# Kernel tuning notes

Hardware: AMD Instinct MI355X
Metric: run time of the kernel (lower is better)

The kernel has to match this reference:

```python
import jax, jax.numpy as jnp
import numpy as np

NUM_GROUPS = 512   # G: number of FPS centers
GROUP_SIZE = 32    # K: neighbors per group


def setup_inputs() -> dict:
    key = jax.random.key(0)
    points = jax.random.normal(key, (16, 8192, 6), dtype=jnp.float32)  # [B,N,C], xyz = first 3 ch
    return {"points": points}


def _farthest_point_sampling(xyz, K):
    """Iterative FPS. xyz: [B,N,3] -> indices [B,K] (int32).

    Deterministic start at index 0 (the torch module uses a random start; we fix
    it for a reproducible reference -- the math per step is identical).
    """
    B, N, _ = xyz.shape
    start = jnp.zeros((B,), dtype=jnp.int32)
    min_d = jnp.full((B, N), jnp.inf, dtype=xyz.dtype)

    def step(carry, _):
        min_d, last = carry
        last_pt = jnp.take_along_axis(xyz, last[:, None, None], axis=1)  # [B,1,3]
        d = jnp.sum((xyz - last_pt) ** 2, axis=-1)                       # [B,N]
        min_d = jnp.minimum(min_d, d)
        nxt = jnp.argmax(min_d, axis=-1).astype(jnp.int32)
        return (min_d, nxt), last

    _, idxs = jax.lax.scan(step, (min_d, start), None, length=K)
    return jnp.transpose(idxs)  # [B,K]


def reference(points):
    xyz = points[:, :, :3]                                   # [B,N,3]
    fps_idx = _farthest_point_sampling(xyz, NUM_GROUPS)      # [B,G]
    centers = jnp.take_along_axis(xyz, fps_idx[:, :, None], axis=1)  # [B,G,3]

    # Squared pairwise distances [B,G,N] via expanded GEMM (compute-dominant part).
    d2 = (jnp.sum(centers * centers, axis=-1)[:, :, None]
          - 2.0 * jnp.einsum('bgc,bnc->bgn', centers, xyz)
          + jnp.sum(xyz * xyz, axis=-1)[:, None, :])

    # KNN: smallest K distances (torch uses return_sorted=False; ordering of the
    # K neighbors is irrelevant to the grouping semantics).
    _, knn_idx = jax.lax.top_k(-d2, GROUP_SIZE)              # [B,G,K]

    # knn_gather: [B,N,C] gathered by [B,G,K] -> [B,G,K,C]
    grouped = jax.vmap(lambda p, i: p[i])(points, knn_idx)

    # Center-subtract on xyz channels only.
    grouped = jnp.concatenate(
        [grouped[..., :3] - centers[:, :, None, :], grouped[..., 3:]], axis=-1)
    return grouped, centers
```

## Files before the change

### kernel.cpp

```cpp
#include <hip/hip_runtime.h>
#include <hip/hip_bf16.h>
#include <stdint.h>

#define BATCH 16
#define NPTS  8192
#define NCH   6
#define NGRP  512
#define GSZ   32

#define FPS_T   1024
#define FPS_PPT 8
#define FPS_W   16

typedef float v2f __attribute__((ext_vector_type(2)));

template <int CTRL>
__device__ __forceinline__ float dpp_max_f32(float v) {
  const int t =
      __builtin_amdgcn_update_dpp(0, __float_as_int(v), CTRL, 0xf, 0xf, true);
  return fmaxf(v, __int_as_float(t));
}

template <int CTRL>
__device__ __forceinline__ unsigned dpp_min_u32(unsigned v) {
  const int t = __builtin_amdgcn_update_dpp((int)0xFFFFFFFF, (int)v, CTRL,
                                            0xf, 0xf, false);
  const unsigned tu = (unsigned)t;
  return v < tu ? v : tu;
}

__global__ __launch_bounds__(FPS_T, 1) void fps_kernel(
    const float* __restrict__ points, float* __restrict__ centers) {
#pragma clang fp contract(off)
  const int b    = blockIdx.x;
  const int tid  = threadIdx.x;
  const int lane = tid & 63;
  const int wave = tid >> 6;
  const float* P = points + (size_t)b * NPTS * NCH;
  float* C = centers + (size_t)b * NGRP * 3;

  __shared__ float cache[NPTS * 3];
  __shared__ unsigned long long wslot[2][FPS_W];

  v2f px[4], py[4], pz[4], md[4];
  {
    float* fx = (float*)px; float* fy = (float*)py; float* fz = (float*)pz;
#pragma unroll
    for (int j = 0; j < FPS_PPT; ++j) {
      const int i = tid * FPS_PPT + j;
      const float x = P[i * 6 + 0];
      const float y = P[i * 6 + 1];
      const float z = P[i * 6 + 2];
      fx[j] = x; fy[j] = y; fz[j] = z;
      cache[i * 3 + 0] = x;
      cache[i * 3 + 1] = y;
      cache[i * 3 + 2] = z;
    }
#pragma unroll
    for (int j = 0; j < 4; ++j) md[j] = (v2f){__builtin_inff(), __builtin_inff()};
  }
  __syncthreads();

  float lx = cache[0], ly = cache[1], lz = cache[2];

  for (int k = 1; k < NGRP; ++k) {
    if (tid == 0) {
      C[(k - 1) * 3 + 0] = lx; C[(k - 1) * 3 + 1] = ly; C[(k - 1) * 3 + 2] = lz;
    }

    const v2f vlx = {lx, lx}, vly = {ly, ly}, vlz = {lz, lz};
    v2f b2 = {-__builtin_inff(), -__builtin_inff()};
#pragma unroll
    for (int j = 0; j < 4; ++j) {
      const v2f dx = px[j] - vlx;
      const v2f dy = py[j] - vly;
      const v2f dz = pz[j] - vlz;
      const v2f d  = (dx * dx + dy * dy) + dz * dz;
      md[j] = __builtin_elementwise_min(md[j], d);
      b2 = __builtin_elementwise_max(b2, md[j]);
    }
    const float bestv = fmaxf(b2.x, b2.y);

    unsigned idxbest = 0;
#pragma unroll
    for (int j = 3; j >= 0; --j) {
      idxbest = (md[j].y == bestv) ? (unsigned)(tid * 8 + 2 * j + 1) : idxbest;
      idxbest = (md[j].x == bestv) ? (unsigned)(tid * 8 + 2 * j)     : idxbest;
    }

    float wv = bestv;
    wv = dpp_max_f32<0x111>(wv); wv = dpp_max_f32<0x112>(wv);
    wv = dpp_max_f32<0x114>(wv); wv = dpp_max_f32<0x118>(wv);
    wv = dpp_max_f32<0x142>(wv); wv = dpp_max_f32<0x143>(wv);
    const float wvmax =
        __int_as_float(__builtin_amdgcn_readlane(__float_as_int(wv), 63));

    const unsigned long long m1 = __ballot(bestv == wvmax);
    const int owner = (int)__builtin_ctzll(m1);
    if (lane == owner)
      wslot[k & 1][wave] =
          ((unsigned long long)__float_as_uint(wvmax) << 32) | idxbest;
    __syncthreads();

    const unsigned long long slot = wslot[k & 1][lane & 15];
    const unsigned sidx = (unsigned)(slot & 0xFFFFFFFFull);
    const float    sval = __uint_as_float((unsigned)(slot >> 32));
    const float ccx = cache[sidx * 3 + 0];
    const float ccy = cache[sidx * 3 + 1];
    const float ccz = cache[sidx * 3 + 2];

    float r = sval;
    r = dpp_max_f32<0x111>(r); r = dpp_max_f32<0x112>(r);
    r = dpp_max_f32<0x114>(r); r = dpp_max_f32<0x118>(r);
    const float gmax =
        __int_as_float(__builtin_amdgcn_readlane(__float_as_int(r), 15));
    const int sstar =
        (int)__builtin_ctzll(__ballot(sval == gmax) & 0xFFFFull);
    lx = __int_as_float(__builtin_amdgcn_readlane(__float_as_int(ccx), sstar));
    ly = __int_as_float(__builtin_amdgcn_readlane(__float_as_int(ccy), sstar));
    lz = __int_as_float(__builtin_amdgcn_readlane(__float_as_int(ccz), sstar));
  }
  if (tid == 0) {
    C[(NGRP - 1) * 3 + 0] = lx;
    C[(NGRP - 1) * 3 + 1] = ly;
    C[(NGRP - 1) * 3 + 2] = lz;
  }
}

__global__ __launch_bounds__(256) void knn_kernel(
    const float* __restrict__ points, const float* __restrict__ centers,
    float* __restrict__ grouped) {
#pragma clang fp contract(off)
  const int g    = blockIdx.x;
  const int b    = blockIdx.y;
  const int tid  = threadIdx.x;
  const int lane = tid & 63;
  const int wave = tid >> 6;
  const float* P   = points + (size_t)b * NPTS * NCH;
  const float* cen = centers + ((size_t)b * NGRP + g) * 3;
  const float cx = cen[0], cy = cen[1], cz = cen[2];
  const float cc = (cx * cx + cy * cy) + cz * cz;

  unsigned long long keys[32];
#pragma unroll
  for (int j = 0; j < 32; ++j) {
    const int i = j * 256 + tid;
    const float2 xy = *reinterpret_cast<const float2*>(P + (size_t)i * 6);
    const float x = xy.x, y = xy.y;
    const float z = P[i * 6 + 2];
    const float xx  = (x * x + y * y) + z * z;
    const float dot = fmaf(cz, z, fmaf(cy, y, cx * x));
    const float d2  = (cc - 2.0f * dot) + xx;
    unsigned u = __float_as_uint(d2);
    u = (u & 0x80000000u) ? ~u : (u | 0x80000000u);
    keys[j] = ((unsigned long long)u << 32) | (unsigned long long)(unsigned)i;
  }

  unsigned long long gm[4];
#pragma unroll
  for (int g2 = 0; g2 < 4; ++g2) {
    unsigned long long m = keys[g2 * 8];
#pragma unroll
    for (int t = 1; t < 8; ++t) {
      const unsigned long long o = keys[g2 * 8 + t];
      m = m < o ? m : o;
    }
    gm[g2] = m;
  }
  unsigned long long lmin;
  {
    const unsigned long long a2 = gm[0] < gm[1] ? gm[0] : gm[1];
    const unsigned long long b3 = gm[2] < gm[3] ? gm[2] : gm[3];
    lmin = a2 < b3 ? a2 : b3;
  }

  __shared__ unsigned long long wtop[4][GSZ];
  __shared__ int knn_sh[GSZ];

  for (int r2 = 0; r2 < GSZ; ++r2) {
    const unsigned vcur = (unsigned)(lmin >> 32);
    const unsigned icur = (unsigned)(lmin & 0xFFFFFFFFull);
    unsigned vm = vcur;
    vm = dpp_min_u32<0x111>(vm); vm = dpp_min_u32<0x112>(vm);
    vm = dpp_min_u32<0x114>(vm); vm = dpp_min_u32<0x118>(vm);
    vm = dpp_min_u32<0x142>(vm); vm = dpp_min_u32<0x143>(vm);
    const unsigned vmin = (unsigned)__builtin_amdgcn_readlane((int)vm, 63);
    unsigned ic = (vcur == vmin) ? icur : 0xFFFFFFFFu;
    ic = dpp_min_u32<0x111>(ic); ic = dpp_min_u32<0x112>(ic);
    ic = dpp_min_u32<0x114>(ic); ic = dpp_min_u32<0x118>(ic);
    ic = dpp_min_u32<0x142>(ic); ic = dpp_min_u32<0x143>(ic);
    const unsigned imin = (unsigned)__builtin_amdgcn_readlane((int)ic, 63);
    const unsigned long long wk =
        ((unsigned long long)vmin << 32) | (unsigned long long)imin;

    if (lane == (int)(imin & 63u)) {
#pragma unroll
      for (int g2 = 0; g2 < 4; ++g2) {
        if (gm[g2] == wk) {
          unsigned long long m = ~0ull;
#pragma unroll
          for (int t = 0; t < 8; ++t) {
            const int s = g2 * 8 + t;
            if (keys[s] == wk) keys[s] = ~0ull;
            const unsigned long long o = keys[s];
            m = m < o ? m : o;
          }
          gm[g2] = m;
        }
      }
      const unsigned long long a2 = gm[0] < gm[1] ? gm[0] : gm[1];
      const unsigned long long b3 = gm[2] < gm[3] ? gm[2] : gm[3];
      lmin = a2 < b3 ? a2 : b3;
    }
    if (lane == 0) wtop[wave][r2] = wk;
  }
  __syncthreads();

  if (wave == 0) {
    const unsigned long long* flat = &wtop[0][0];
    unsigned long long a = flat[lane];
    unsigned long long c = flat[lane + 64];
#pragma unroll
    for (int k2 = 2; k2 <= 128; k2 <<= 1) {
#pragma unroll
      for (int j2 = k2 >> 1; j2 >= 1; j2 >>= 1) {
        if (j2 == 64) {
          const unsigned long long mn = a < c ? a : c;
          const unsigned long long mx = a < c ? c : a;
          a = mn; c = mx;
        } else {
          const bool upa = ((lane & k2) == 0);
          const bool upc = (((lane + 64) & k2) == 0);
          const unsigned long long oa = __shfl_xor(a, j2);
          const unsigned long long oc = __shfl_xor(c, j2);
          const bool low = ((lane & j2) == 0);
          const unsigned long long mna = a < oa ? a : oa;
          const unsigned long long mxa = a < oa ? oa : a;
          const unsigned long long mnc = c < oc ? c : oc;
          const unsigned long long mxc = c < oc ? oc : c;
          a = (low == upa) ? mna : mxa;
          c = (low == upc) ? mnc : mxc;
        }
      }
    }
    if (lane < GSZ) knn_sh[lane] = (int)(unsigned)(a & 0xFFFFFFFFull);
  }
  __syncthreads();

  float* outg = grouped + ((size_t)b * NGRP + g) * GSZ * NCH;
  for (int t = tid; t < GSZ * NCH; t += 256) {
    const int n = t / 6, c2 = t % 6;
    const int idx = knn_sh[n];
    float v = P[idx * 6 + c2];
    if (c2 < 3) v = v - cen[c2];
    outg[t] = v;
  }
}

extern "C" void kernel_launch(void* const* d_in, const int* in_sizes, int n_in,
                              void* d_out, int out_size, void* d_ws, size_t ws_size,
                              hipStream_t stream) {
  const float* points = (const float*)d_in[0];
  float* out = (float*)d_out;
  float* grouped = out;
  float* centers = out + (size_t)BATCH * NGRP * GSZ * NCH;

  fps_kernel<<<BATCH, FPS_T, 0, stream>>>(points, centers);
  knn_kernel<<<dim3(NGRP, BATCH), 256, 0, stream>>>(points, centers, grouped);
}
```

Baseline: 741.7 us.

## Fuse FPS and KNN into one persistent kernel with progress-flag streaming

Merges the FPS and KNN kernels into a single launch. Blocks take a ticket from an atomic counter: the first 16 run FPS and publish progress every 8 centers with release stores, and the rest run KNN for 4 groups each, spin-waiting until the centers they need exist. KNN work can then overlap the long serial FPS loop instead of waiting for it to finish. The cost is a memset launch, spin-polling, and a larger 1024-thread block for KNN, with a risk of starving the FPS blocks for CU resources.

```diff
diff --git a/kernel.cpp b/kernel.cpp
--- a/kernel.cpp
+++ b/kernel.cpp
@@ -8,9 +8,11 @@
 #define NGRP  512
 #define GSZ   32
 
-#define FPS_T   1024
+#define TPB    1024
 #define FPS_PPT 8
 #define FPS_W   16
+#define GPB     4
+#define KNB     (BATCH * NGRP / GPB)
 
 typedef float v2f __attribute__((ext_vector_type(2)));
 
@@ -29,231 +31,266 @@
   return v < tu ? v : tu;
 }
 
-__global__ __launch_bounds__(FPS_T, 1) void fps_kernel(
-    const float* __restrict__ points, float* __restrict__ centers) {
+__global__ __launch_bounds__(TPB, 1) void fused_kernel(
+    const float* __restrict__ points, float* __restrict__ grouped,
+    float* __restrict__ centers, unsigned* __restrict__ ws) {
 #pragma clang fp contract(off)
-  const int b    = blockIdx.x;
+  __shared__ union {
+    struct {
+      float cache[NPTS * 3];
+      unsigned long long wslot[2][FPS_W];
+    } f;
+    struct {
+      unsigned long long wtop[16][GSZ];
+      int knn_sh[GPB][GSZ];
+    } k;
+  } u;
+  __shared__ unsigned ticket_sh;
+
   const int tid  = threadIdx.x;
   const int lane = tid & 63;
   const int wave = tid >> 6;
-  const float* P = points + (size_t)b * NPTS * NCH;
-  float* C = centers + (size_t)b * NGRP * 3;
-
-  __shared__ float cache[NPTS * 3];
-  __shared__ unsigned long long wslot[2][FPS_W];
-
-  v2f px[4], py[4], pz[4], md[4];
-  {
-    float* fx = (float*)px; float* fy = (float*)py; float* fz = (float*)pz;
-#pragma unroll
-    for (int j = 0; j < FPS_PPT; ++j) {
-      const int i = tid * FPS_PPT + j;
-      const float x = P[i * 6 + 0];
-      const float y = P[i * 6 + 1];
+
+  if (tid == 0) ticket_sh = atomicAdd(ws, 1u);
+  __syncthreads();
+  const unsigned ticket = ticket_sh;
+
+  if (ticket < BATCH) {
+    const int b = (int)ticket;
+    const float* P = points + (size_t)b * NPTS * NCH;
+    float* C = centers + (size_t)b * NGRP * 3;
+    unsigned* prog = ws + 32 + b * 32;
+
+    v2f px[4], py[4], pz[4], md[4];
+    {
+      float* fx = (float*)px; float* fy = (float*)py; float* fz = (float*)pz;
+#pragma unroll
+      for (int j = 0; j < FPS_PPT; ++j) {
+        const int i = tid * FPS_PPT + j;
+        const float x = P[i * 6 + 0];
+        const float y = P[i * 6 + 1];
+        const float z = P[i * 6 + 2];
+        fx[j] = x; fy[j] = y; fz[j] = z;
+        u.f.cache[i * 3 + 0] = x;
+        u.f.cache[i * 3 + 1] = y;
+        u.f.cache[i * 3 + 2] = z;
+      }
+#pragma unroll
+      for (int j = 0; j < 4; ++j)
+        md[j] = (v2f){__builtin_inff(), __builtin_inff()};
+    }
+    __syncthreads();
+
+    float lx = u.f.cache[0], ly = u.f.cache[1], lz = u.f.cache[2];
+
+    for (int k = 1; k < NGRP; ++k) {
+      if (tid == 0) {
+        C[(k - 1) * 3 + 0] = lx;
+        C[(k - 1) * 3 + 1] = ly;
+        C[(k - 1) * 3 + 2] = lz;
+        if ((k & 7) == 0)
+          __hip_atomic_store(prog, (unsigned)k, __ATOMIC_RELEASE,
+                             __HIP_MEMORY_SCOPE_AGENT);
+      }
+
+      const v2f vlx = {lx, lx}, vly = {ly, ly}, vlz = {lz, lz};
+      v2f b2 = {-__builtin_inff(), -__builtin_inff()};
+#pragma unroll
+      for (int j = 0; j < 4; ++j) {
+        const v2f dx = px[j] - vlx;
+        const v2f dy = py[j] - vly;
+        const v2f dz = pz[j] - vlz;
+        const v2f d  = (dx * dx + dy * dy) + dz * dz;
+        md[j] = __builtin_elementwise_min(md[j], d);
+        b2 = __builtin_elementwise_max(b2, md[j]);
+      }
+      const float bestv = fmaxf(b2.x, b2.y);
+
+      unsigned idxbest = 0;
+#pragma unroll
+      for (int j = 3; j >= 0; --j) {
+        idxbest = (md[j].y == bestv) ? (unsigned)(tid * 8 + 2 * j + 1) : idxbest;
+        idxbest = (md[j].x == bestv) ? (unsigned)(tid * 8 + 2 * j)     : idxbest;
+      }
+
+      float wv = bestv;
+      wv = dpp_max_f32<0x111>(wv); wv = dpp_max_f32<0x112>(wv);
+      wv = dpp_max_f32<0x114>(wv); wv = dpp_max_f32<0x118>(wv);
+      wv = dpp_max_f32<0x142>(wv); wv = dpp_max_f32<0x143>(wv);
+      const float wvmax =
+          __int_as_float(__builtin_amdgcn_readlane(__float_as_int(wv), 63));
+      const int owner = (int)__builtin_ctzll(__ballot(bestv == wvmax));
+      if (lane == owner)
+        u.f.wslot[k & 1][wave] =
+            ((unsigned long long)__float_as_uint(wvmax) << 32) | idxbest;
+      __syncthreads();
+
+      const unsigned long long slot = u.f.wslot[k & 1][lane & 15];
+      const unsigned sidx = (unsigned)(slot & 0xFFFFFFFFull);
+      const float    sval = __uint_as_float((unsigned)(slot >> 32));
+      const float ccx = u.f.cache[sidx * 3 + 0];
+      const float ccy = u.f.cache[sidx * 3 + 1];
+      const float ccz = u.f.cache[sidx * 3 + 2];
+
+      float r = sval;
+      r = dpp_max_f32<0x111>(r); r = dpp_max_f32<0x112>(r);
+      r = dpp_max_f32<0x114>(r); r = dpp_max_f32<0x118>(r);
+      const float gmax =
+          __int_as_float(__builtin_amdgcn_readlane(__float_as_int(r), 15));
+      const int sstar =
+          (int)__builtin_ctzll(__ballot(sval == gmax) & 0xFFFFull);
+      lx = __int_as_float(__builtin_amdgcn_readlane(__float_as_int(ccx), sstar));
+      ly = __int_as_float(__builtin_amdgcn_readlane(__float_as_int(ccy), sstar));
+      lz = __int_as_float(__builtin_amdgcn_readlane(__float_as_int(ccz), sstar));
+    }
+    if (tid == 0) {
+      C[(NGRP - 1) * 3 + 0] = lx;
+      C[(NGRP - 1) * 3 + 1] = ly;
+      C[(NGRP - 1) * 3 + 2] = lz;
+      __hip_atomic_store(prog, (unsigned)NGRP, __ATOMIC_RELEASE,
+                         __HIP_MEMORY_SCOPE_AGENT);
+    }
+  } else {
+    const unsigned gid = ticket - BATCH;
+    const int b  = (int)(gid & 15);
+    const int g0 = (int)(gid >> 4) * GPB;
+    const int sub  = tid >> 8;
+    const int t256 = tid & 255;
+    const int g = g0 + sub;
+    const float* P = points + (size_t)b * NPTS * NCH;
+    const float* cen = centers + ((size_t)b * NGRP + g) * 3;
+    unsigned* prog = ws + 32 + b * 32;
+
+    if (tid == 0) {
+      while (__hip_atomic_load(prog, __ATOMIC_ACQUIRE,
+                               __HIP_MEMORY_SCOPE_AGENT) <
+             (unsigned)(g0 + GPB))
+        __builtin_amdgcn_s_sleep(16);
+    }
+    __syncthreads();
+
+    const float cx = __hip_atomic_load(&cen[0], __ATOMIC_RELAXED,
+                                       __HIP_MEMORY_SCOPE_AGENT);
+    const float cy = __hip_atomic_load(&cen[1], __ATOMIC_RELAXED,
+                                       __HIP_MEMORY_SCOPE_AGENT);
+    const float cz = __hip_atomic_load(&cen[2], __ATOMIC_RELAXED,
+                                       __HIP_MEMORY_SCOPE_AGENT);
+    const float cc = (cx * cx + cy * cy) + cz * cz;
+
+    unsigned long long keys[32];
+#pragma unroll
+    for (int j = 0; j < 32; ++j) {
+      const int i = j * 256 + t256;
+      const float2 xy = *reinterpret_cast<const float2*>(P + (size_t)i * 6);
+      const float x = xy.x, y = xy.y;
       const float z = P[i * 6 + 2];
-      fx[j] = x; fy[j] = y; fz[j] = z;
-      cache[i * 3 + 0] = x;
-      cache[i * 3 + 1] = y;
-      cache[i * 3 + 2] = z;
-    }
-#pragma unroll
-    for (int j = 0; j < 4; ++j) md[j] = (v2f){__builtin_inff(), __builtin_inff()};
-  }
-  __syncthreads();
-
-  float lx = cache[0], ly = cache[1], lz = cache[2];
-
-  for (int k = 1; k < NGRP; ++k) {
-    if (tid == 0) {
-      C[(k - 1) * 3 + 0] = lx; C[(k - 1) * 3 + 1] = ly; C[(k - 1) * 3 + 2] = lz;
-    }
-
-    const v2f vlx = {lx, lx}, vly = {ly, ly}, vlz = {lz, lz};
-    v2f b2 = {-__builtin_inff(), -__builtin_inff()};
-#pragma unroll
-    for (int j = 0; j < 4; ++j) {
-      const v2f dx = px[j] - vlx;
-      const v2f dy = py[j] - vly;
-      const v2f dz = pz[j] - vlz;
-      const v2f d  = (dx * dx + dy * dy) + dz * dz;
-      md[j] = __builtin_elementwise_min(md[j], d);
-      b2 = __builtin_elementwise_max(b2, md[j]);
-    }
-    const float bestv = fmaxf(b2.x, b2.y);
-
-    unsigned idxbest = 0;
-#pragma unroll
-    for (int j = 3; j >= 0; --j) {
-      idxbest = (md[j].y == bestv) ? (unsigned)(tid * 8 + 2 * j + 1) : idxbest;
-      idxbest = (md[j].x == bestv) ? (unsigned)(tid * 8 + 2 * j)     : idxbest;
-    }
-
-    float wv = bestv;
-    wv = dpp_max_f32<0x111>(wv); wv = dpp_max_f32<0x112>(wv);
-    wv = dpp_max_f32<0x114>(wv); wv = dpp_max_f32<0x118>(wv);
-    wv = dpp_max_f32<0x142>(wv); wv = dpp_max_f32<0x143>(wv);
-    const float wvmax =
-        __int_as_float(__builtin_amdgcn_readlane(__float_as_int(wv), 63));
-
-    const unsigned long long m1 = __ballot(bestv == wvmax);
-    const int owner = (int)__builtin_ctzll(m1);
-    if (lane == owner)
-      wslot[k & 1][wave] =
-          ((unsigned long long)__float_as_uint(wvmax) << 32) | idxbest;
-    __syncthreads();
-
-    const unsigned long long slot = wslot[k & 1][lane & 15];
-    const unsigned sidx = (unsigned)(slot & 0xFFFFFFFFull);
-    const float    sval = __uint_as_float((unsigned)(slot >> 32));
-    const float ccx = cache[sidx * 3 + 0];
-    const float ccy = cache[sidx * 3 + 1];
-    const float ccz = cache[sidx * 3 + 2];
-
-    float r = sval;
-    r = dpp_max_f32<0x111>(r); r = dpp_max_f32<0x112>(r);
-    r = dpp_max_f32<0x114>(r); r = dpp_max_f32<0x118>(r);
-    const float gmax =
-        __int_as_float(__builtin_amdgcn_readlane(__float_as_int(r), 15));
-    const int sstar =
-        (int)__builtin_ctzll(__ballot(sval == gmax) & 0xFFFFull);
-    lx = __int_as_float(__builtin_amdgcn_readlane(__float_as_int(ccx), sstar));
-    ly = __int_as_float(__builtin_amdgcn_readlane(__float_as_int(ccy), sstar));
-    lz = __int_as_float(__builtin_amdgcn_readlane(__float_as_int(ccz), sstar));
-  }
-  if (tid == 0) {
-    C[(NGRP - 1) * 3 + 0] = lx;
-    C[(NGRP - 1) * 3 + 1] = ly;
-    C[(NGRP - 1) * 3 + 2] = lz;
-  }
-}
-
-__global__ __launch_bounds__(256) void knn_kernel(
-    const float* __restrict__ points, const float* __restrict__ centers,
-    float* __restrict__ grouped) {
-#pragma clang fp contract(off)
-  const int g    = blockIdx.x;
-  const int b    = blockIdx.y;
-  const int tid  = threadIdx.x;
-  const int lane = tid & 63;
-  const int wave = tid >> 6;
-  const float* P   = points + (size_t)b * NPTS * NCH;
-  const float* cen = centers + ((size_t)b * NGRP + g) * 3;
-  const float cx = cen[0], cy = cen[1], cz = cen[2];
-  const float cc = (cx * cx + cy * cy) + cz * cz;
-
-  unsigned long long keys[32];
-#pragma unroll
-  for (int j = 0; j < 32; ++j) {
-    const int i = j * 256 + tid;
-    const float2 xy = *reinterpret_cast<const float2*>(P + (size_t)i * 6);
-    const float x = xy.x, y = xy.y;
-    const float z = P[i * 6 + 2];
-    const float xx  = (x * x + y * y) + z * z;
-    const float dot = fmaf(cz, z, fmaf(cy, y, cx * x));
-    const float d2  = (cc - 2.0f * dot) + xx;
-    unsigned u = __float_as_uint(d2);
-    u = (u & 0x80000000u) ? ~u : (u | 0x80000000u);
-    keys[j] = ((unsigned long long)u << 32) | (unsigned long long)(unsigned)i;
-  }
-
-  unsigned long long gm[4];
-#pragma unroll
-  for (int g2 = 0; g2 < 4; ++g2) {
-    unsigned long long m = keys[g2 * 8];
-#pragma unroll
-    for (int t = 1; t < 8; ++t) {
-      const unsigned long long o = keys[g2 * 8 + t];
-      m = m < o ? m : o;
-    }
-    gm[g2] = m;
-  }
-  unsigned long long lmin;
-  {
-    const unsigned long long a2 = gm[0] < gm[1] ? gm[0] : gm[1];
-    const unsigned long long b3 = gm[2] < gm[3] ? gm[2] : gm[3];
-    lmin = a2 < b3 ? a2 : b3;
-  }
-
-  __shared__ unsigned long long wtop[4][GSZ];
-  __shared__ int knn_sh[GSZ];
-
-  for (int r2 = 0; r2 < GSZ; ++r2) {
-    const unsigned vcur = (unsigned)(lmin >> 32);
-    const unsigned icur = (unsigned)(lmin & 0xFFFFFFFFull);
-    unsigned vm = vcur;
-    vm = dpp_min_u32<0x111>(vm); vm = dpp_min_u32<0x112>(vm);
-    vm = dpp_min_u32<0x114>(vm); vm = dpp_min_u32<0x118>(vm);
-    vm = dpp_min_u32<0x142>(vm); vm = dpp_min_u32<0x143>(vm);
-    const unsigned vmin = (unsigned)__builtin_amdgcn_readlane((int)vm, 63);
-    unsigned ic = (vcur == vmin) ? icur : 0xFFFFFFFFu;
-    ic = dpp_min_u32<0x111>(ic); ic = dpp_min_u32<0x112>(ic);
-    ic = dpp_min_u32<0x114>(ic); ic = dpp_min_u32<0x118>(ic);
-    ic = dpp_min_u32<0x142>(ic); ic = dpp_min_u32<0x143>(ic);
-    const unsigned imin = (unsigned)__builtin_amdgcn_readlane((int)ic, 63);
-    const unsigned long long wk =
-        ((unsigned long long)vmin << 32) | (unsigned long long)imin;
-
-    if (lane == (int)(imin & 63u)) {
-#pragma unroll
-      for (int g2 = 0; g2 < 4; ++g2) {
-        if (gm[g2] == wk) {
-          unsigned long long m = ~0ull;
-#pragma unroll
-          for (int t = 0; t < 8; ++t) {
-            const int s = g2 * 8 + t;
-            if (keys[s] == wk) keys[s] = ~0ull;
-            const unsigned long long o = keys[s];
-            m = m < o ? m : o;
-          }
-          gm[g2] = m;
-        }
-      }
+      const float xx  = (x * x + y * y) + z * z;
+      const float dot = fmaf(cz, z, fmaf(cy, y, cx * x));
+      const float d2  = (cc - 2.0f * dot) + xx;
+      unsigned uu = __float_as_uint(d2);
+      uu = (uu & 0x80000000u) ? ~uu : (uu | 0x80000000u);
+      keys[j] = ((unsigned long long)uu << 32) | (unsigned long long)(unsigned)i;
+    }
+
+    unsigned long long gm[4];
+#pragma unroll
+    for (int g2 = 0; g2 < 4; ++g2) {
+      unsigned long long m = keys[g2 * 8];
+#pragma unroll
+      for (int t = 1; t < 8; ++t) {
+        const unsigned long long o = keys[g2 * 8 + t];
+        m = m < o ? m : o;
+      }
+      gm[g2] = m;
+    }
+    unsigned long long lmin;
+    {
       const unsigned long long a2 = gm[0] < gm[1] ? gm[0] : gm[1];
       const unsigned long long b3 = gm[2] < gm[3] ? gm[2] : gm[3];
       lmin = a2 < b3 ? a2 : b3;
     }
-    if (lane == 0) wtop[wave][r2] = wk;
-  }
-  __syncthreads();
-
-  if (wave == 0) {
-    const unsigned long long* flat = &wtop[0][0];
-    unsigned long long a = flat[lane];
-    unsigned long long c = flat[lane + 64];
-#pragma unroll
-    for (int k2 = 2; k2 <= 128; k2 <<= 1) {
-#pragma unroll
-      for (int j2 = k2 >> 1; j2 >= 1; j2 >>= 1) {
-        if (j2 == 64) {
-          const unsigned long long mn = a < c ? a : c;
-          const unsigned long long mx = a < c ? c : a;
-          a = mn; c = mx;
-        } else {
-          const bool upa = ((lane & k2) == 0);
-          const bool upc = (((lane + 64) & k2) == 0);
-          const unsigned long long oa = __shfl_xor(a, j2);
-          const unsigned long long oc = __shfl_xor(c, j2);
-          const bool low = ((lane & j2) == 0);
-          const unsigned long long mna = a < oa ? a : oa;
-          const unsigned long long mxa = a < oa ? oa : a;
-          const unsigned long long mnc = c < oc ? c : oc;
-          const unsigned long long mxc = c < oc ? oc : c;
-          a = (low == upa) ? mna : mxa;
-          c = (low == upc) ? mnc : mxc;
+
+    for (int r2 = 0; r2 < GSZ; ++r2) {
+      const unsigned vcur = (unsigned)(lmin >> 32);
+      const unsigned icur = (unsigned)(lmin & 0xFFFFFFFFull);
+      unsigned vm = vcur;
+      vm = dpp_min_u32<0x111>(vm); vm = dpp_min_u32<0x112>(vm);
+      vm = dpp_min_u32<0x114>(vm); vm = dpp_min_u32<0x118>(vm);
+      vm = dpp_min_u32<0x142>(vm); vm = dpp_min_u32<0x143>(vm);
+      const unsigned vmin = (unsigned)__builtin_amdgcn_readlane((int)vm, 63);
+      unsigned ic = (vcur == vmin) ? icur : 0xFFFFFFFFu;
+      ic = dpp_min_u32<0x111>(ic); ic = dpp_min_u32<0x112>(ic);
+      ic = dpp_min_u32<0x114>(ic); ic = dpp_min_u32<0x118>(ic);
+      ic = dpp_min_u32<0x142>(ic); ic = dpp_min_u32<0x143>(ic);
+      const unsigned imin = (unsigned)__builtin_amdgcn_readlane((int)ic, 63);
+      const unsigned long long wk =
+          ((unsigned long long)vmin << 32) | (unsigned long long)imin;
+
+      if (lane == (int)(imin & 63u)) {
+#pragma unroll
+        for (int g2 = 0; g2 < 4; ++g2) {
+          if (gm[g2] == wk) {
+            unsigned long long m = ~0ull;
+#pragma unroll
+            for (int t = 0; t < 8; ++t) {
+              const int s = g2 * 8 + t;
+              if (keys[s] == wk) keys[s] = ~0ull;
+              const unsigned long long o = keys[s];
+              m = m < o ? m : o;
+            }
+            gm[g2] = m;
+          }
         }
-      }
-    }
-    if (lane < GSZ) knn_sh[lane] = (int)(unsigned)(a & 0xFFFFFFFFull);
-  }
-  __syncthreads();
-
-  float* outg = grouped + ((size_t)b * NGRP + g) * GSZ * NCH;
-  for (int t = tid; t < GSZ * NCH; t += 256) {
-    const int n = t / 6, c2 = t % 6;
-    const int idx = knn_sh[n];
-    float v = P[idx * 6 + c2];
-    if (c2 < 3) v = v - cen[c2];
-    outg[t] = v;
+        const unsigned long long a2 = gm[0] < gm[1] ? gm[0] : gm[1];
+        const unsigned long long b3 = gm[2] < gm[3] ? gm[2] : gm[3];
+        lmin = a2 < b3 ? a2 : b3;
+      }
+      if (lane == 0) u.k.wtop[wave][r2] = wk;
+    }
+    __syncthreads();
+
+    if ((wave & 3) == 0) {
+      const unsigned long long* flat = &u.k.wtop[4 * sub][0];
+      unsigned long long a = flat[lane];
+      unsigned long long c = flat[lane + 64];
+#pragma unroll
+      for (int k2 = 2; k2 <= 128; k2 <<= 1) {
+#pragma unroll
+        for (int j2 = k2 >> 1; j2 >= 1; j2 >>= 1) {
+          if (j2 == 64) {
+            const unsigned long long mn = a < c ? a : c;
+            const unsigned long long mx = a < c ? c : a;
+            a = mn; c = mx;
+          } else {
+            const bool upa = ((lane & k2) == 0);
+            const bool upc = (((lane + 64) & k2) == 0);
+            const unsigned long long oa = __shfl_xor(a, j2);
+            const unsigned long long oc = __shfl_xor(c, j2);
+            const bool low = ((lane & j2) == 0);
+            const unsigned long long mna = a < oa ? a : oa;
+            const unsigned long long mxa = a < oa ? oa : a;
+            const unsigned long long mnc = c < oc ? c : oc;
+            const unsigned long long mxc = c < oc ? oc : c;
+            a = (low == upa) ? mna : mxa;
+            c = (low == upc) ? mnc : mxc;
+          }
+        }
+      }
+      if (lane < GSZ) u.k.knn_sh[sub][lane] = (int)(unsigned)(a & 0xFFFFFFFFull);
+    }
+    __syncthreads();
+
+    float* outg = grouped + ((size_t)b * NGRP + g) * GSZ * NCH;
+    if (t256 < GSZ * NCH) {
+      const int n = t256 / 6, c2 = t256 % 6;
+      const int idx = u.k.knn_sh[sub][n];
+      float v = P[idx * 6 + c2];
+      if (c2 < 3) {
+        const float cv = (c2 == 0) ? cx : (c2 == 1) ? cy : cz;
+        v = v - cv;
+      }
+      outg[t256] = v;
+    }
   }
 }
 
@@ -264,7 +301,8 @@
   float* out = (float*)d_out;
   float* grouped = out;
   float* centers = out + (size_t)BATCH * NGRP * GSZ * NCH;
-
-  fps_kernel<<<BATCH, FPS_T, 0, stream>>>(points, centers);
-  knn_kernel<<<dim3(NGRP, BATCH), 256, 0, stream>>>(points, centers, grouped);
+  unsigned* ws = (unsigned*)d_ws;
+
+  hipMemsetAsync(ws, 0, 4096, stream);
+  fused_kernel<<<BATCH + KNB, TPB, 0, stream>>>(points, grouped, centers, ws);
 }
```

Result: no change. 733.1 us (-1.2%).
